# Kernel optimization log

Measured on AMD Instinct MI355X. Metric: run time of the kernel, lower is better.

The kernel has to match this reference:

```python
import jax, jax.numpy as jnp
import numpy as np

HEADS = 2
OUT_CH = 128
NEG_SLOPE_ATT = 0.2   # GATv2Conv attention LeakyReLU
NEG_SLOPE_ACT = 0.01  # nn.LeakyReLU default
BN_EPS = 1e-5


def setup_inputs() -> dict:
    key = jax.random.key(0)
    ks = jax.random.split(key, 8)
    B, C, D, H, W = 2, 128, 8, 32, 32
    N = B * D * H * W            # 16384 graph nodes
    E = 196608                   # avg degree 12
    x = jax.random.normal(ks[0], (B, C, D, H, W), dtype=jnp.float32)
    edge_index = jax.random.randint(ks[1], (2, E), 0, N, dtype=jnp.int64)
    lin_w = jax.random.normal(ks[2], (C, HEADS * OUT_CH), dtype=jnp.float32) * (1.0 / np.sqrt(C))
    lin_b = jax.random.normal(ks[3], (HEADS * OUT_CH,), dtype=jnp.float32) * 0.02
    att = jax.random.normal(ks[4], (HEADS, OUT_CH), dtype=jnp.float32) * (1.0 / np.sqrt(OUT_CH))
    gat_bias = jax.random.normal(ks[5], (OUT_CH,), dtype=jnp.float32) * 0.02
    bn_gamma = jnp.ones((OUT_CH,), dtype=jnp.float32)
    bn_beta = jnp.zeros((OUT_CH,), dtype=jnp.float32)
    return {"x": x, "edge_index": edge_index, "lin_w": lin_w, "lin_b": lin_b,
            "att": att, "gat_bias": gat_bias, "bn_gamma": bn_gamma, "bn_beta": bn_beta}


def _gatv2(xf, src, dst, lin_w, lin_b, att, gat_bias, n_nodes):
    # shared-weights GATv2: x' = x W + b, per edge e=(j->i): score = a . lrelu(x'_i + x'_j)
    h = (xf @ lin_w + lin_b).reshape(n_nodes, HEADS, OUT_CH)  # [N, H, C]
    x_src = h[src]                                            # [E, H, C] messages
    logits = jnp.einsum('ehc,hc->eh', jax.nn.leaky_relu(x_src + h[dst], NEG_SLOPE_ATT), att)
    # segment softmax over edges sharing the same target node
    m = jax.ops.segment_max(logits, dst, num_segments=n_nodes)      # [N, H]
    ex = jnp.exp(logits - m[dst])
    denom = jax.ops.segment_sum(ex, dst, num_segments=n_nodes)      # [N, H]
    alpha = ex / denom[dst]
    out = jax.ops.segment_sum(x_src * alpha[..., None], dst, num_segments=n_nodes)  # [N, H, C]
    return out.mean(axis=1) + gat_bias  # concat=False -> head mean


def reference(x, edge_index, lin_w, lin_b, att, gat_bias, bn_gamma, bn_beta):
    B, C, D, H, W = x.shape
    N = B * D * H * W
    xf = x.reshape(B, C, -1).transpose(0, 2, 1).reshape(N, C)
    # add_self_loops=True (PyG default)
    loop = jnp.arange(N, dtype=edge_index.dtype)
    src = jnp.concatenate([edge_index[0], loop])
    dst = jnp.concatenate([edge_index[1], loop])
    out = _gatv2(xf, src, dst, lin_w, lin_b, att, gat_bias, N)      # [N, OUT_CH]
    out = out.reshape(B, D * H * W, OUT_CH).transpose(0, 2, 1).reshape(B, OUT_CH, D, H, W)
    # BatchNorm3d (training-mode batch stats, biased variance)
    mean = out.mean(axis=(0, 2, 3, 4), keepdims=True)
    var = out.var(axis=(0, 2, 3, 4), keepdims=True)
    out = (out - mean) / jnp.sqrt(var + BN_EPS)
    out = out * bn_gamma.reshape(1, -1, 1, 1, 1) + bn_beta.reshape(1, -1, 1, 1, 1)
    return jax.nn.leaky_relu(out, NEG_SLOPE_ACT)
```

## Files before the change

### kernel.cpp

```cpp
#include <hip/hip_runtime.h>
#include <math.h>

#define N_NODES 16384
#define CIN 128
#define HOUT 256
#define OUTC 128
#define NEG_ATT 0.2f
#define NEG_ACT 0.01f
#define BN_EPS 1e-5f
#define ELLW 64

typedef short short8 __attribute__((ext_vector_type(8)));
typedef float f32x4 __attribute__((ext_vector_type(4)));

static __device__ __forceinline__ unsigned short f2bf(float f) {
    unsigned int u = __float_as_uint(f);
    unsigned int r = (u + 0x7FFFu + ((u >> 16) & 1u)) >> 16;
    return (unsigned short)r;
}
static __device__ __forceinline__ void loadbf8(const unsigned short* p, float* f) {
    uint4 u = *(const uint4*)p;
    f[0] = __uint_as_float(u.x << 16);
    f[1] = __uint_as_float(u.x & 0xffff0000u);
    f[2] = __uint_as_float(u.y << 16);
    f[3] = __uint_as_float(u.y & 0xffff0000u);
    f[4] = __uint_as_float(u.z << 16);
    f[5] = __uint_as_float(u.z & 0xffff0000u);
    f[6] = __uint_as_float(u.w << 16);
    f[7] = __uint_as_float(u.w & 0xffff0000u);
}
template <int CTRL>
static __device__ __forceinline__ float dppadd(float x) {
    return x + __int_as_float(__builtin_amdgcn_update_dpp(
        0, __float_as_int(x), CTRL, 0xF, 0xF, true));
}
#define DPP_XOR1 0xB1
#define DPP_XOR2 0x4E
#define DPP_HMIR 0x141
#define DPP_MIR  0x140

#define LDP 136
__global__ __launch_bounds__(256) void gemm_kernel(const float* __restrict__ x,
                                                   const float* __restrict__ lin_w,
                                                   const float* __restrict__ lin_b,
                                                   unsigned short* __restrict__ h,
                                                   int* __restrict__ deg,
                                                   float* __restrict__ gz) {
    __shared__ __align__(16) unsigned short A_s[64 * LDP];
    __shared__ __align__(16) unsigned short Bt_s[64 * LDP];
    const int t = threadIdx.x;
    const int bid = blockIdx.x;

    if (t < 16) deg[bid * 16 + t] = 0;
    if (bid == 0) gz[t] = 0.f;

    const int node0 = (bid >> 2) * 64;
    const int o0 = (bid & 3) * 64;
    const int b = node0 >> 13;
    const int s0 = node0 & 8191;

    const int nt = t & 15;
    const int kt = t >> 4;
#pragma unroll
    for (int p = 0; p < 2; p++) {
        const int kb = p * 64 + kt * 4;
        float4 ar[4], br[4];
#pragma unroll
        for (int r = 0; r < 4; r++) {
            ar[r] = *(const float4*)&x[((b * CIN + kb + r) << 13) + s0 + nt * 4];
            br[r] = *(const float4*)&lin_w[(kb + r) * HOUT + o0 + nt * 4];
        }
#pragma unroll
        for (int j = 0; j < 4; j++) {
            ushort4 va, vb;
            va.x = f2bf(((const float*)&ar[0])[j]);
            va.y = f2bf(((const float*)&ar[1])[j]);
            va.z = f2bf(((const float*)&ar[2])[j]);
            va.w = f2bf(((const float*)&ar[3])[j]);
            vb.x = f2bf(((const float*)&br[0])[j]);
            vb.y = f2bf(((const float*)&br[1])[j]);
            vb.z = f2bf(((const float*)&br[2])[j]);
            vb.w = f2bf(((const float*)&br[3])[j]);
            *(ushort4*)&A_s[(nt * 4 + j) * LDP + kb] = va;
            *(ushort4*)&Bt_s[(nt * 4 + j) * LDP + kb] = vb;
        }
    }
    __syncthreads();

    const int w = t >> 6;
    const int lane = t & 63;
    const int lrow = lane & 15;
    const int lquad = lane >> 4;
    const int m0 = w * 16;

    short8 afr[4];
#pragma unroll
    for (int ks = 0; ks < 4; ks++)
        afr[ks] = *(const short8*)&A_s[(m0 + lrow) * LDP + ks * 32 + lquad * 8];

    f32x4 acc[4];
#pragma unroll
    for (int c = 0; c < 4; c++) { acc[c][0] = 0.f; acc[c][1] = 0.f; acc[c][2] = 0.f; acc[c][3] = 0.f; }

#pragma unroll
    for (int c = 0; c < 4; c++) {
#pragma unroll
        for (int ks = 0; ks < 4; ks++) {
            short8 bfr = *(const short8*)&Bt_s[(c * 16 + lrow) * LDP + ks * 32 + lquad * 8];
            acc[c] = __builtin_amdgcn_mfma_f32_16x16x32_bf16(afr[ks], bfr, acc[c], 0, 0, 0);
        }
    }

#pragma unroll
    for (int c = 0; c < 4; c++) {
        const int col = o0 + c * 16 + lrow;
        const float lb = lin_b[col];
#pragma unroll
        for (int r = 0; r < 4; r++) {
            const int n = node0 + m0 + lquad * 4 + r;
            h[n * HOUT + col] = f2bf(acc[c][r] + lb);
        }
    }
}

__global__ void ell_scatter_kernel(const int* __restrict__ edges, int* __restrict__ deg,
                                   int* __restrict__ ell, int E) {
    int e = blockIdx.x * 256 + threadIdx.x;
    if (e < E) {
        int s = edges[e];
        int d = edges[E + e];
        int slot = atomicAdd(&deg[d], 1);
        if (slot < ELLW) ell[(d << 6) + slot] = s;
    }
}

__global__ __launch_bounds__(256) void gat_kernel(const unsigned short* __restrict__ h,
                                                  const int* __restrict__ deg,
                                                  const int* __restrict__ ell,
                                                  const float* __restrict__ att,
                                                  const float* __restrict__ gat_bias,
                                                  float* __restrict__ gat,
                                                  float* __restrict__ gsum,
                                                  float* __restrict__ gsumsq) {
    const int t = threadIdx.x;
    const int lane = t & 63;
    const int w = t >> 6;
    const int half = lane >> 5;
    const int sub = lane & 31;
    const int c0 = sub * 8;

    __shared__ float ssum[128], ssq[128];
    if (t < 128) { ssum[t] = 0.f; ssq[t] = 0.f; }
    __syncthreads();

    float av[8];
    *(float4*)&av[0] = *(const float4*)&att[c0];
    *(float4*)&av[4] = *(const float4*)&att[c0 + 4];
    float gb[8];
    *(float4*)&gb[0] = *(const float4*)&gat_bias[c0 & 127];
    *(float4*)&gb[4] = *(const float4*)&gat_bias[(c0 & 127) + 4];

    float st[8] = {}, sq[8] = {};

    for (int i = 0; i < 4; i++) {
        const int node = (blockIdx.x << 4) + (w << 2) + i;
        float hd[8];
        loadbf8(&h[node * HOUT + c0], hd);
        const int dN = deg[node];
        const int cnt = (dN < ELLW ? dN : ELLW) + 1;
        const int* __restrict__ row = &ell[node << 6];
        float denom = 0.f;
        float acc[8] = {};

        for (int base = 0; base < cnt; base += 8) {
            int ei[4], jj[4];
#pragma unroll
            for (int u = 0; u < 4; u++) {
                ei[u] = base + 2 * u + half;
                jj[u] = (ei[u] == 0) ? node : ((ei[u] < cnt) ? row[ei[u] - 1] : node);
            }
            float hj[4][8];
#pragma unroll
            for (int u = 0; u < 4; u++)
                loadbf8(&h[jj[u] * HOUT + c0], hj[u]);
            float p[4];
#pragma unroll
            for (int u = 0; u < 4; u++) {
                float d = 0.f;
#pragma unroll
                for (int c = 0; c < 8; c++) {
                    float v = hj[u][c] + hd[c];
                    v = fmaxf(v, NEG_ATT * v);
                    d = fmaf(v, av[c], d);
                }
                p[u] = d;
            }
#pragma unroll
            for (int u = 0; u < 4; u++) p[u] = dppadd<DPP_XOR1>(p[u]);
#pragma unroll
            for (int u = 0; u < 4; u++) p[u] = dppadd<DPP_XOR2>(p[u]);
#pragma unroll
            for (int u = 0; u < 4; u++) p[u] = dppadd<DPP_HMIR>(p[u]);
#pragma unroll
            for (int u = 0; u < 4; u++) p[u] = dppadd<DPP_MIR>(p[u]);
#pragma unroll
            for (int u = 0; u < 4; u++) {
                float wt = (ei[u] < cnt) ? __expf(p[u]) : 0.f;
                denom += wt;
#pragma unroll
                for (int c = 0; c < 8; c++) acc[c] = fmaf(wt, hj[u][c], acc[c]);
            }
        }
        denom += __shfl_xor(denom, 32);
#pragma unroll
        for (int c = 0; c < 8; c++) acc[c] += __shfl_xor(acc[c], 32);
        float inv = 1.0f / denom;
        float r[8];
#pragma unroll
        for (int c = 0; c < 8; c++) r[c] = acc[c] * inv;
#pragma unroll
        for (int c = 0; c < 8; c++) r[c] += __shfl_xor(r[c], 16);
        if (lane < 16) {
            float o[8];
#pragma unroll
            for (int c = 0; c < 8; c++) {
                o[c] = 0.5f * r[c] + gb[c];
                st[c] += o[c];
                sq[c] += o[c] * o[c];
            }
            *(float4*)&gat[node * OUTC + c0] = *(float4*)&o[0];
            *(float4*)&gat[node * OUTC + c0 + 4] = *(float4*)&o[4];
        }
    }
    if (lane < 16) {
#pragma unroll
        for (int c = 0; c < 8; c++) {
            atomicAdd(&ssum[c0 + c], st[c]);
            atomicAdd(&ssq[c0 + c], sq[c]);
        }
    }
    __syncthreads();
    if (t < 128) {
        atomicAdd(&gsum[t], ssum[t]);
        atomicAdd(&gsumsq[t], ssq[t]);
    }
}

__global__ __launch_bounds__(256) void epilogue_kernel(const float* __restrict__ gat,
                                                       const float* __restrict__ gsum,
                                                       const float* __restrict__ gsumsq,
                                                       const float* __restrict__ gamma,
                                                       const float* __restrict__ beta,
                                                       float* __restrict__ out) {
    __shared__ float tile[64 * 129];
    __shared__ float sc[128], sh[128];
    const int t = threadIdx.x;
    if (t < 128) {
        const float invN = 1.0f / (float)N_NODES;
        float mean = gsum[t] * invN;
        float var = gsumsq[t] * invN - mean * mean;
        float rstd = rsqrtf(var + BN_EPS);
        float s = gamma[t] * rstd;
        sc[t] = s;
        sh[t] = beta[t] - mean * s;
    }
    __syncthreads();
    const int n0 = blockIdx.x * 64;
    const int b = n0 >> 13;
    const int s0 = n0 & 8191;
#pragma unroll
    for (int k = 0; k < 32; k++) {
        int f = t + k * 256;
        int nl = f >> 7;
        int c = f & 127;
        float v = gat[(n0 << 7) + f];
        v = v * sc[c] + sh[c];
        v = v > 0.f ? v : NEG_ACT * v;
        tile[nl * 129 + c] = v;
    }
    __syncthreads();
    const int sl = t & 63;
    const int c0 = t >> 6;
#pragma unroll
    for (int k = 0; k < 32; k++) {
        int c = c0 + (k << 2);
        out[((b * OUTC + c) << 13) + s0 + sl] = tile[sl * 129 + c];
    }
}

extern "C" void kernel_launch(void* const* d_in, const int* in_sizes, int n_in,
                              void* d_out, int out_size, void* d_ws, size_t ws_size,
                              hipStream_t stream) {
    const float* x        = (const float*)d_in[0];
    const int*   edges    = (const int*)d_in[1];
    const float* lin_w    = (const float*)d_in[2];
    const float* lin_b    = (const float*)d_in[3];
    const float* att      = (const float*)d_in[4];
    const float* gat_bias = (const float*)d_in[5];
    const float* bn_gamma = (const float*)d_in[6];
    const float* bn_beta  = (const float*)d_in[7];
    float* out = (float*)d_out;
    int E = in_sizes[1] / 2;

    char* ws = (char*)d_ws;
    unsigned short* h = (unsigned short*)(ws);
    float* gat     = (float*)(ws + 8388608);
    int*   deg     = (int*)(ws + 16777216);
    int*   ell     = (int*)(ws + 16842752);
    float* gsum    = (float*)(ws + 21037056);
    float* gsumsq  = gsum + 128;

    gemm_kernel<<<1024, 256, 0, stream>>>(x, lin_w, lin_b, h, deg, gsum);
    ell_scatter_kernel<<<(E + 255) / 256, 256, 0, stream>>>(edges, deg, ell, E);
    gat_kernel<<<N_NODES / 16, 256, 0, stream>>>(h, deg, ell, att, gat_bias, gat, gsum, gsumsq);
    epilogue_kernel<<<N_NODES / 64, 256, 0, stream>>>(gat, gsum, gsumsq, bn_gamma, bn_beta, out);
}
```

Measured before the change: 138.5 us.

## Fuse ELL scatter into GEMM launch and prefetch next neighbor indices

The edge-to-ELL scatter now runs as extra blocks of the GEMM kernel, so the two independent stages share one launch and can overlap. Zeroing the degree array moves to a hipMemsetAsync before that launch. The GAT loop now loads the next batch of neighbor indices one iteration ahead, to hide the latency of the dependent index-then-row gather. The cost is an extra memset launch, and the scatter blocks' shared-memory allocation may limit how many of them run at once.

```diff
diff --git a/kernel.cpp b/kernel.cpp
--- a/kernel.cpp
+++ b/kernel.cpp
@@ -9,6 +9,7 @@
 #define NEG_ACT 0.01f
 #define BN_EPS 1e-5f
 #define ELLW 64
+#define GEMM_BLOCKS 1024
 
 typedef short short8 __attribute__((ext_vector_type(8)));
 typedef float f32x4 __attribute__((ext_vector_type(4)));
@@ -40,18 +41,30 @@
 #define DPP_MIR  0x140
 
 #define LDP 136
-__global__ __launch_bounds__(256) void gemm_kernel(const float* __restrict__ x,
-                                                   const float* __restrict__ lin_w,
-                                                   const float* __restrict__ lin_b,
-                                                   unsigned short* __restrict__ h,
-                                                   int* __restrict__ deg,
-                                                   float* __restrict__ gz) {
+__global__ __launch_bounds__(256) void gemm_scatter_kernel(const float* __restrict__ x,
+                                                           const float* __restrict__ lin_w,
+                                                           const float* __restrict__ lin_b,
+                                                           unsigned short* __restrict__ h,
+                                                           const int* __restrict__ edges,
+                                                           int* __restrict__ deg,
+                                                           int* __restrict__ ell,
+                                                           float* __restrict__ gz, int E) {
     __shared__ __align__(16) unsigned short A_s[64 * LDP];
     __shared__ __align__(16) unsigned short Bt_s[64 * LDP];
     const int t = threadIdx.x;
     const int bid = blockIdx.x;
 
-    if (t < 16) deg[bid * 16 + t] = 0;
+    if (bid >= GEMM_BLOCKS) {
+        int e = (bid - GEMM_BLOCKS) * 256 + t;
+        if (e < E) {
+            int s = edges[e];
+            int d = edges[E + e];
+            int slot = atomicAdd(&deg[d], 1);
+            if (slot < ELLW) ell[(d << 6) + slot] = s;
+        }
+        return;
+    }
+
     if (bid == 0) gz[t] = 0.f;
 
     const int node0 = (bid >> 2) * 64;
@@ -120,17 +133,6 @@
             const int n = node0 + m0 + lquad * 4 + r;
             h[n * HOUT + col] = f2bf(acc[c][r] + lb);
         }
-    }
-}
-
-__global__ void ell_scatter_kernel(const int* __restrict__ edges, int* __restrict__ deg,
-                                   int* __restrict__ ell, int E) {
-    int e = blockIdx.x * 256 + threadIdx.x;
-    if (e < E) {
-        int s = edges[e];
-        int d = edges[E + e];
-        int slot = atomicAdd(&deg[d], 1);
-        if (slot < ELLW) ell[(d << 6) + slot] = s;
     }
 }
 
@@ -172,17 +174,26 @@
         float denom = 0.f;
         float acc[8] = {};
 
+        int jn[4];
+#pragma unroll
+        for (int u = 0; u < 4; u++) {
+            int e = 2 * u + half;
+            jn[u] = (e == 0) ? node : ((e < cnt) ? row[e - 1] : node);
+        }
+
         for (int base = 0; base < cnt; base += 8) {
-            int ei[4], jj[4];
+            int jc[4];
+#pragma unroll
+            for (int u = 0; u < 4; u++) jc[u] = jn[u];
 #pragma unroll
             for (int u = 0; u < 4; u++) {
-                ei[u] = base + 2 * u + half;
-                jj[u] = (ei[u] == 0) ? node : ((ei[u] < cnt) ? row[ei[u] - 1] : node);
+                int e = base + 8 + 2 * u + half;
+                jn[u] = (e < cnt) ? row[e - 1] : node;
             }
             float hj[4][8];
 #pragma unroll
             for (int u = 0; u < 4; u++)
-                loadbf8(&h[jj[u] * HOUT + c0], hj[u]);
+                loadbf8(&h[jc[u] * HOUT + c0], hj[u]);
             float p[4];
 #pragma unroll
             for (int u = 0; u < 4; u++) {
@@ -205,7 +216,7 @@
             for (int u = 0; u < 4; u++) p[u] = dppadd<DPP_MIR>(p[u]);
 #pragma unroll
             for (int u = 0; u < 4; u++) {
-                float wt = (ei[u] < cnt) ? __expf(p[u]) : 0.f;
+                float wt = ((base + 2 * u + half) < cnt) ? __expf(p[u]) : 0.f;
                 denom += wt;
 #pragma unroll
                 for (int c = 0; c < 8; c++) acc[c] = fmaf(wt, hj[u][c], acc[c]);
@@ -310,8 +321,10 @@
     float* gsum    = (float*)(ws + 21037056);
     float* gsumsq  = gsum + 128;
 
-    gemm_kernel<<<1024, 256, 0, stream>>>(x, lin_w, lin_b, h, deg, gsum);
-    ell_scatter_kernel<<<(E + 255) / 256, 256, 0, stream>>>(edges, deg, ell, E);
+    hipMemsetAsync(deg, 0, N_NODES * sizeof(int), stream);
+    const int scatter_blocks = (E + 255) / 256;
+    gemm_scatter_kernel<<<GEMM_BLOCKS + scatter_blocks, 256, 0, stream>>>(
+        x, lin_w, lin_b, h, edges, deg, ell, gsum, E);
     gat_kernel<<<N_NODES / 16, 256, 0, stream>>>(h, deg, ell, att, gat_bias, gat, gsum, gsumsq);
     epilogue_kernel<<<N_NODES / 64, 256, 0, stream>>>(gat, gsum, gsumsq, bn_gamma, bn_beta, out);
 }
```

Result: faster. 134.6 us (median of 2 runs) (-2.8%).
